# Performance work log

Hardware: AMD Instinct MI355X
Metric: run time of the kernel (lower is better)

The kernel has to match this reference:

```python
import jax, jax.numpy as jnp
import numpy as np

B, C, D, H, W = 2, 64, 8, 24, 24  # hidden_dim = C; N = D*H*W = 4608 tokens


def setup_inputs() -> dict:
    key = jax.random.key(0)
    ks = jax.random.split(key, 8)
    s = 1.0 / np.sqrt(C)  # fan-in style init for 1x1 conv weights
    return {
        "x": jax.random.normal(ks[0], (B, C, D, H, W), dtype=jnp.float32),
        "h": jax.random.normal(ks[1], (B, C, D, H, W), dtype=jnp.float32),
        "Wq": jax.random.normal(ks[2], (C, C), dtype=jnp.float32) * s,
        "bq": jax.random.normal(ks[3], (C,), dtype=jnp.float32) * s,
        "Wk": jax.random.normal(ks[4], (C, C), dtype=jnp.float32) * s,
        "bk": jax.random.normal(ks[5], (C,), dtype=jnp.float32) * s,
        "Wv": jax.random.normal(ks[6], (C, C), dtype=jnp.float32) * s,
        "bv": jax.random.normal(ks[7], (C,), dtype=jnp.float32) * s,
    }


def reference(x, h, Wq, bq, Wk, bk, Wv, bv):
    # 1x1 Conv3d == per-token linear over channels
    def proj(inp, Wt, bt):
        f = inp.reshape(inp.shape[0], inp.shape[1], -1)  # [B, C, N]
        return jnp.einsum('oc,bcn->bon', Wt, f) + bt[None, :, None]

    q = proj(x, Wq, bq)  # [B, C, N]
    k = proj(h, Wk, bk)  # [B, C, N]
    v = proj(h, Wv, bv)  # [B, C, N]

    scale = 1.0 / np.sqrt(k.shape[1])  # k.size(1) ** 0.5 == sqrt(C)
    scores = jnp.einsum('bcm,bcn->bmn', q, k) * scale  # [B, N, N]
    attn = jax.nn.softmax(scores, axis=-1)
    out = jnp.einsum('bcn,bmn->bcm', v, attn)  # [B, C, N]
    return out.reshape(h.shape)
```

## Files before the change

### kernel.cpp

```cpp
#include <hip/hip_runtime.h>
#include <hip/hip_bf16.h>

#define C_DIM 64
#define N_TOK 4608
#define NBLK  72
#define B_SZ  2
#define MTILES 288
#define NSEG  8
#define SEGLEN (N_TOK / NSEG)
#define KTILES 288
#define VTILES 72

typedef __bf16 bf16x8 __attribute__((ext_vector_type(8)));
typedef float  f32x4  __attribute__((ext_vector_type(4)));


__device__ __forceinline__ void gemm_tile(
    const __hip_bfloat16* wmat, const bf16x8 bin[2], const float* bias,
    int col, int quad, f32x4 acc[4])
{
    #pragma unroll
    for (int ot = 0; ot < 4; ot++) {
        f32x4 a = (f32x4){0.f, 0.f, 0.f, 0.f};
        #pragma unroll
        for (int kh = 0; kh < 2; kh++) {
            bf16x8 wf = *(const bf16x8*)(wmat + (ot * 16 + col) * 72 +
                                         kh * 32 + quad * 8);
            a = __builtin_amdgcn_mfma_f32_16x16x32_bf16(wf, bin[kh], a, 0, 0, 0);
        }
        float4 b4 = *(const float4*)(bias + ot * 16 + quad * 4);
        a[0] += b4.x; a[1] += b4.y; a[2] += b4.z; a[3] += b4.w;
        acc[ot] = a;
    }
}

__device__ __forceinline__ void store_swz(
    __hip_bfloat16* dst, const f32x4 acc[4], int col, int quad, float sc)
{
    #pragma unroll
    for (int ot = 0; ot < 4; ot++) {
        union { __hip_bfloat16 e[4]; uint2 v; } pk;
        #pragma unroll
        for (int r = 0; r < 4; r++) pk.e[r] = __float2bfloat16(acc[ot][r] * sc);
        *(uint2*)(dst + (ot >> 1) * 512 + ((ot * 2 + (quad >> 1)) & 3) * 128 +
                  col * 8 + (quad & 1) * 4) = pk.v;
    }
}

__global__ __launch_bounds__(256) void proj_kernel(
    const float* __restrict__ x,  const float* __restrict__ h,
    const float* __restrict__ Wq, const float* __restrict__ bq,
    const float* __restrict__ Wk, const float* __restrict__ bk,
    const float* __restrict__ Wv, const float* __restrict__ bv,
    __hip_bfloat16* __restrict__ qS, __hip_bfloat16* __restrict__ kS,
    __hip_bfloat16* __restrict__ vS)
{
    __shared__ __hip_bfloat16 wl[3 * 64 * 72];
    __shared__ __hip_bfloat16 xt[64 * 72];
    __shared__ __hip_bfloat16 ht[64 * 72];
    __shared__ __hip_bfloat16 vl[64 * 72];

    const int b  = blockIdx.x / NBLK;
    const int n0 = (blockIdx.x % NBLK) * 64;
    const int t  = threadIdx.x;

    #pragma unroll
    for (int mat = 0; mat < 3; mat++) {
        const float* W = (mat == 0) ? Wq : ((mat == 1) ? Wk : Wv);
        __hip_bfloat16* wd = wl + mat * (64 * 72);
        #pragma unroll
        for (int i = 0; i < 16; i++) {
            const int idx = i * 256 + t;
            wd[(idx >> 6) * 72 + (idx & 63)] = __float2bfloat16(W[idx]);
        }
    }
    #pragma unroll
    for (int i = 0; i < 16; i++) {
        const int idx = i * 256 + t;
        const int c = idx >> 6, n = idx & 63;
        xt[n * 72 + c] = __float2bfloat16(x[(size_t)(b * C_DIM + c) * N_TOK + n0 + n]);
        ht[n * 72 + c] = __float2bfloat16(h[(size_t)(b * C_DIM + c) * N_TOK + n0 + n]);
    }
    __syncthreads();

    const int wave = t >> 6, lane = t & 63;
    const int col = lane & 15, quad = lane >> 4;

    bf16x8 xb[2], hb[2];
    #pragma unroll
    for (int kh = 0; kh < 2; kh++) {
        xb[kh] = *(const bf16x8*)(xt + (wave * 16 + col) * 72 + kh * 32 + quad * 8);
        hb[kh] = *(const bf16x8*)(ht + (wave * 16 + col) * 72 + kh * 32 + quad * 8);
    }

    const size_t tile16 = (size_t)b * KTILES + (n0 >> 4) + wave;
    f32x4 acc[4];

    gemm_tile(wl + 0 * (64 * 72), xb, bq, col, quad, acc);
    store_swz(qS + (tile16 << 10), acc, col, quad, 0.125f * 1.44269504088896f);

    gemm_tile(wl + 1 * (64 * 72), hb, bk, col, quad, acc);
    store_swz(kS + (tile16 << 10), acc, col, quad, 1.0f);

    gemm_tile(wl + 2 * (64 * 72), hb, bv, col, quad, acc);
    #pragma unroll
    for (int ot = 0; ot < 4; ot++)
        #pragma unroll
        for (int r = 0; r < 4; r++)
            vl[(ot * 16 + quad * 4 + r) * 72 + wave * 16 + col] =
                __float2bfloat16(acc[ot][r]);
    __syncthreads();
    {
        const size_t vbase = ((size_t)(b * VTILES) + (n0 >> 6)) << 12;
        #pragma unroll
        for (int rep = 0; rep < 2; rep++) {
            const int ch = rep * 256 + t;
            const int cc = ch >> 7, hf = (ch >> 6) & 1;
            const int qd = (ch >> 4) & 3, c2 = ch & 15;
            *(uint4*)(vS + vbase + (size_t)ch * 8) =
                *(const uint4*)(vl + (cc * 16 + c2) * 72 + hf * 32 + qd * 8);
        }
    }
}

__global__ __launch_bounds__(512, 4) void attn_kernel(
    const __hip_bfloat16* __restrict__ qS,
    const __hip_bfloat16* __restrict__ kS,
    const __hip_bfloat16* __restrict__ vS,
    float* __restrict__ out)
{
    __shared__ __hip_bfloat16 plds[NSEG * 16 * 72];
    __shared__ float o_lds[NSEG * 16 * 64];
    __shared__ float mstat[NSEG][16];
    __shared__ float lstat[NSEG][16];

    const int b    = blockIdx.x / MTILES;
    const int mblk = blockIdx.x % MTILES;
    const int wave = threadIdx.x >> 6;
    const int lane = threadIdx.x & 63;
    const int col  = lane & 15;
    const int quad = lane >> 4;
    const int m0   = mblk * 16;

    __hip_bfloat16* pw = plds + wave * (16 * 72);

    const __hip_bfloat16* qp =
        qS + (((size_t)b * KTILES + (m0 >> 4)) << 10) + lane * 8;
    const bf16x8 qf0 = *(const bf16x8*)(qp);
    const bf16x8 qf1 = *(const bf16x8*)(qp + 512);

    f32x4 accO[4];
    #pragma unroll
    for (int cc = 0; cc < 4; cc++) accO[cc] = (f32x4){0.f, 0.f, 0.f, 0.f};
    float rmax = -3.0e38f, rsum = 0.f;

    const int nbeg = wave * SEGLEN;

    #pragma unroll 1
    for (int n0 = nbeg; n0 < nbeg + SEGLEN; n0 += 64) {
        const __hip_bfloat16* vt =
            vS + ((((size_t)b * VTILES) + (n0 >> 6)) << 12) + lane * 8;
        bf16x8 va[8];
        #pragma unroll
        for (int cc = 0; cc < 4; cc++) {
            va[2 * cc]     = *(const bf16x8*)(vt + cc * 1024);
            va[2 * cc + 1] = *(const bf16x8*)(vt + cc * 1024 + 512);
        }

        const __hip_bfloat16* kt =
            kS + (((size_t)b * KTILES + (n0 >> 4)) << 10) + lane * 8;
        f32x4 s[4];
        #pragma unroll
        for (int j = 0; j < 4; j++) {
            bf16x8 ka0 = *(const bf16x8*)(kt + (j << 10));
            bf16x8 ka1 = *(const bf16x8*)(kt + (j << 10) + 512);
            s[j] = __builtin_amdgcn_mfma_f32_16x16x32_bf16(
                       ka0, qf0, (f32x4){0.f, 0.f, 0.f, 0.f}, 0, 0, 0);
            s[j] = __builtin_amdgcn_mfma_f32_16x16x32_bf16(ka1, qf1, s[j], 0, 0, 0);
        }

        float tm = s[0][0];
        #pragma unroll
        for (int j = 0; j < 4; j++)
            #pragma unroll
            for (int r = 0; r < 4; r++) tm = fmaxf(tm, s[j][r]);
        tm = fmaxf(tm, __shfl_xor(tm, 16));
        tm = fmaxf(tm, __shfl_xor(tm, 32));
        const float nmax  = fmaxf(rmax, tm);
        const float alpha = __builtin_amdgcn_exp2f(rmax - nmax);
        rmax = nmax;

        float pv[16];
        float psum = 0.f;
        #pragma unroll
        for (int j = 0; j < 4; j++)
            #pragma unroll
            for (int r = 0; r < 4; r++) {
                float e = __builtin_amdgcn_exp2f(s[j][r] - nmax);
                pv[j * 4 + r] = e;
                psum += e;
            }
        rsum = rsum * alpha + psum;

        #pragma unroll
        for (int cc = 0; cc < 4; cc++)
            #pragma unroll
            for (int r = 0; r < 4; r++) accO[cc][r] *= alpha;

        #pragma unroll
        for (int j = 0; j < 4; j++) {
            union { __hip_bfloat16 e[4]; uint2 v; } pk;
            #pragma unroll
            for (int r = 0; r < 4; r++) pk.e[r] = __float2bfloat16(pv[j * 4 + r]);
            *(uint2*)(pw + col * 72 + j * 16 + quad * 4) = pk.v;
        }
        __asm__ volatile("s_waitcnt lgkmcnt(0)" ::: "memory");

        const bf16x8 pb0 = *(const bf16x8*)(pw + col * 72 + quad * 8);
        const bf16x8 pb1 = *(const bf16x8*)(pw + col * 72 + 32 + quad * 8);
        #pragma unroll
        for (int cc = 0; cc < 4; cc++) {
            accO[cc] = __builtin_amdgcn_mfma_f32_16x16x32_bf16(va[2 * cc],     pb0, accO[cc], 0, 0, 0);
            accO[cc] = __builtin_amdgcn_mfma_f32_16x16x32_bf16(va[2 * cc + 1], pb1, accO[cc], 0, 0, 0);
        }
    }

    rsum += __shfl_xor(rsum, 16);
    rsum += __shfl_xor(rsum, 32);
    #pragma unroll
    for (int cc = 0; cc < 4; cc++)
        *(f32x4*)(o_lds + (wave * 16 + col) * 64 + cc * 16 + quad * 4) = accO[cc];
    if (quad == 0) { mstat[wave][col] = rmax; lstat[wave][col] = rsum; }
    __syncthreads();

    if (threadIdx.x < 256) {
        const int m  = threadIdx.x & 15;
        const int cq = threadIdx.x >> 4;
        float M = -3.0e38f;
        #pragma unroll
        for (int sgm = 0; sgm < NSEG; sgm++) M = fmaxf(M, mstat[sgm][m]);
        float lsum = 0.f;
        f32x4 oacc = (f32x4){0.f, 0.f, 0.f, 0.f};
        #pragma unroll
        for (int sgm = 0; sgm < NSEG; sgm++) {
            const float w = __builtin_amdgcn_exp2f(mstat[sgm][m] - M);
            lsum += w * lstat[sgm][m];
            oacc += w * *(const f32x4*)(o_lds + (sgm * 16 + m) * 64 + cq * 4);
        }
        const float inv = 1.0f / lsum;
        #pragma unroll
        for (int r = 0; r < 4; r++) {
            const int c = cq * 4 + r;
            out[(size_t)(b * C_DIM + c) * N_TOK + m0 + m] = oacc[r] * inv;
        }
    }
}

extern "C" void kernel_launch(void* const* d_in, const int* in_sizes, int n_in,
                              void* d_out, int out_size, void* d_ws, size_t ws_size,
                              hipStream_t stream) {
    const float* x  = (const float*)d_in[0];
    const float* h  = (const float*)d_in[1];
    const float* Wq = (const float*)d_in[2];
    const float* bq = (const float*)d_in[3];
    const float* Wk = (const float*)d_in[4];
    const float* bk = (const float*)d_in[5];
    const float* Wv = (const float*)d_in[6];
    const float* bv = (const float*)d_in[7];
    float* out = (float*)d_out;

    const size_t elems = (size_t)B_SZ * N_TOK * C_DIM;
    __hip_bfloat16* qS = (__hip_bfloat16*)d_ws;
    __hip_bfloat16* kS = qS + elems;
    __hip_bfloat16* vS = kS + elems;

    proj_kernel<<<B_SZ * NBLK, 256, 0, stream>>>(x, h, Wq, bq, Wk, bk, Wv, bv,
                                                 qS, kS, vS);
    attn_kernel<<<B_SZ * MTILES, 512, 0, stream>>>(qS, kS, vS, out);
}
```

Baseline: 106.6 us.

## Process two query tiles per attention block and vectorize projection loads

Each attention block now handles 32 query rows (two 16-row tiles) instead of 16, so every K and V fragment loaded from global memory feeds twice as many MFMAs. This halves the grid to 288 blocks and raises register pressure from the doubled accumulators and score tiles. The final merge is done in two phases, with an output LDS stride padded to 68 to reduce bank conflicts. The projection kernel switches to float4 global loads for the weights and activations.

```diff
diff --git a/kernel.cpp b/kernel.cpp
--- a/kernel.cpp
+++ b/kernel.cpp
@@ -5,11 +5,12 @@
 #define N_TOK 4608
 #define NBLK  72
 #define B_SZ  2
-#define MTILES 288
+#define MBLKS 144
 #define NSEG  8
 #define SEGLEN (N_TOK / NSEG)
 #define KTILES 288
 #define VTILES 72
+#define OSTR  68
 
 typedef __bf16 bf16x8 __attribute__((ext_vector_type(8)));
 typedef float  f32x4  __attribute__((ext_vector_type(4)));
@@ -69,17 +70,30 @@
         const float* W = (mat == 0) ? Wq : ((mat == 1) ? Wk : Wv);
         __hip_bfloat16* wd = wl + mat * (64 * 72);
         #pragma unroll
-        for (int i = 0; i < 16; i++) {
-            const int idx = i * 256 + t;
-            wd[(idx >> 6) * 72 + (idx & 63)] = __float2bfloat16(W[idx]);
-        }
-    }
-    #pragma unroll
-    for (int i = 0; i < 16; i++) {
-        const int idx = i * 256 + t;
-        const int c = idx >> 6, n = idx & 63;
-        xt[n * 72 + c] = __float2bfloat16(x[(size_t)(b * C_DIM + c) * N_TOK + n0 + n]);
-        ht[n * 72 + c] = __float2bfloat16(h[(size_t)(b * C_DIM + c) * N_TOK + n0 + n]);
+        for (int i = 0; i < 4; i++) {
+            const int ch = i * 256 + t;
+            const int o = ch >> 4, c0 = (ch & 15) * 4;
+            float4 w4 = *(const float4*)(W + ch * 4);
+            union { __hip_bfloat16 e[4]; uint2 v; } pk;
+            pk.e[0] = __float2bfloat16(w4.x); pk.e[1] = __float2bfloat16(w4.y);
+            pk.e[2] = __float2bfloat16(w4.z); pk.e[3] = __float2bfloat16(w4.w);
+            *(uint2*)(wd + o * 72 + c0) = pk.v;
+        }
+    }
+    #pragma unroll
+    for (int i = 0; i < 4; i++) {
+        const int ch = i * 256 + t;
+        const int c = ch >> 4, n4 = (ch & 15) * 4;
+        float4 x4 = *(const float4*)(x + (size_t)(b * C_DIM + c) * N_TOK + n0 + n4);
+        float4 h4 = *(const float4*)(h + (size_t)(b * C_DIM + c) * N_TOK + n0 + n4);
+        xt[(n4 + 0) * 72 + c] = __float2bfloat16(x4.x);
+        xt[(n4 + 1) * 72 + c] = __float2bfloat16(x4.y);
+        xt[(n4 + 2) * 72 + c] = __float2bfloat16(x4.z);
+        xt[(n4 + 3) * 72 + c] = __float2bfloat16(x4.w);
+        ht[(n4 + 0) * 72 + c] = __float2bfloat16(h4.x);
+        ht[(n4 + 1) * 72 + c] = __float2bfloat16(h4.y);
+        ht[(n4 + 2) * 72 + c] = __float2bfloat16(h4.z);
+        ht[(n4 + 3) * 72 + c] = __float2bfloat16(h4.w);
     }
     __syncthreads();
 
@@ -129,35 +143,121 @@
     const __hip_bfloat16* __restrict__ vS,
     float* __restrict__ out)
 {
-    __shared__ __hip_bfloat16 plds[NSEG * 16 * 72];
-    __shared__ float o_lds[NSEG * 16 * 64];
-    __shared__ float mstat[NSEG][16];
-    __shared__ float lstat[NSEG][16];
-
-    const int b    = blockIdx.x / MTILES;
-    const int mblk = blockIdx.x % MTILES;
+    __shared__ __hip_bfloat16 plds[NSEG * 2 * 16 * 72];
+    __shared__ float o_lds[NSEG * 16 * OSTR];
+    __shared__ float mstat[NSEG][32];
+    __shared__ float lstat[NSEG][32];
+
+    const int b    = blockIdx.x / MBLKS;
+    const int mblk = blockIdx.x % MBLKS;
     const int wave = threadIdx.x >> 6;
     const int lane = threadIdx.x & 63;
     const int col  = lane & 15;
     const int quad = lane >> 4;
-    const int m0   = mblk * 16;
-
-    __hip_bfloat16* pw = plds + wave * (16 * 72);
+    const int m0   = mblk * 32;
+
+    __hip_bfloat16* pw0 = plds + wave * (2 * 16 * 72);
+    __hip_bfloat16* pw1 = pw0 + 16 * 72;
 
     const __hip_bfloat16* qp =
         qS + (((size_t)b * KTILES + (m0 >> 4)) << 10) + lane * 8;
-    const bf16x8 qf0 = *(const bf16x8*)(qp);
-    const bf16x8 qf1 = *(const bf16x8*)(qp + 512);
-
-    f32x4 accO[4];
-    #pragma unroll
-    for (int cc = 0; cc < 4; cc++) accO[cc] = (f32x4){0.f, 0.f, 0.f, 0.f};
-    float rmax = -3.0e38f, rsum = 0.f;
+    const bf16x8 qa0 = *(const bf16x8*)(qp);
+    const bf16x8 qa1 = *(const bf16x8*)(qp + 512);
+    const bf16x8 qb0 = *(const bf16x8*)(qp + 1024);
+    const bf16x8 qb1 = *(const bf16x8*)(qp + 1536);
+
+    f32x4 accO0[4], accO1[4];
+    #pragma unroll
+    for (int cc = 0; cc < 4; cc++) {
+        accO0[cc] = (f32x4){0.f, 0.f, 0.f, 0.f};
+        accO1[cc] = (f32x4){0.f, 0.f, 0.f, 0.f};
+    }
+    float rmax0 = -3.0e38f, rsum0 = 0.f;
+    float rmax1 = -3.0e38f, rsum1 = 0.f;
 
     const int nbeg = wave * SEGLEN;
 
     #pragma unroll 1
     for (int n0 = nbeg; n0 < nbeg + SEGLEN; n0 += 64) {
+        const __hip_bfloat16* kt =
+            kS + (((size_t)b * KTILES + (n0 >> 4)) << 10) + lane * 8;
+        bf16x8 ka[8];
+        #pragma unroll
+        for (int j = 0; j < 4; j++) {
+            ka[2 * j]     = *(const bf16x8*)(kt + (j << 10));
+            ka[2 * j + 1] = *(const bf16x8*)(kt + (j << 10) + 512);
+        }
+
+        f32x4 s0[4], s1[4];
+        #pragma unroll
+        for (int j = 0; j < 4; j++) {
+            s0[j] = __builtin_amdgcn_mfma_f32_16x16x32_bf16(
+                        ka[2 * j], qa0, (f32x4){0.f, 0.f, 0.f, 0.f}, 0, 0, 0);
+            s0[j] = __builtin_amdgcn_mfma_f32_16x16x32_bf16(ka[2 * j + 1], qa1, s0[j], 0, 0, 0);
+            s1[j] = __builtin_amdgcn_mfma_f32_16x16x32_bf16(
+                        ka[2 * j], qb0, (f32x4){0.f, 0.f, 0.f, 0.f}, 0, 0, 0);
+            s1[j] = __builtin_amdgcn_mfma_f32_16x16x32_bf16(ka[2 * j + 1], qb1, s1[j], 0, 0, 0);
+        }
+
+        {
+            float tm = s0[0][0];
+            #pragma unroll
+            for (int j = 0; j < 4; j++)
+                #pragma unroll
+                for (int r = 0; r < 4; r++) tm = fmaxf(tm, s0[j][r]);
+            tm = fmaxf(tm, __shfl_xor(tm, 16));
+            tm = fmaxf(tm, __shfl_xor(tm, 32));
+            const float nmax  = fmaxf(rmax0, tm);
+            const float alpha = __builtin_amdgcn_exp2f(rmax0 - nmax);
+            rmax0 = nmax;
+            float psum = 0.f;
+            #pragma unroll
+            for (int j = 0; j < 4; j++) {
+                union { __hip_bfloat16 e[4]; uint2 v; } pk;
+                #pragma unroll
+                for (int r = 0; r < 4; r++) {
+                    float e = __builtin_amdgcn_exp2f(s0[j][r] - nmax);
+                    psum += e;
+                    pk.e[r] = __float2bfloat16(e);
+                }
+                *(uint2*)(pw0 + col * 72 + j * 16 + quad * 4) = pk.v;
+            }
+            rsum0 = rsum0 * alpha + psum;
+            #pragma unroll
+            for (int cc = 0; cc < 4; cc++)
+                #pragma unroll
+                for (int r = 0; r < 4; r++) accO0[cc][r] *= alpha;
+        }
+        {
+            float tm = s1[0][0];
+            #pragma unroll
+            for (int j = 0; j < 4; j++)
+                #pragma unroll
+                for (int r = 0; r < 4; r++) tm = fmaxf(tm, s1[j][r]);
+            tm = fmaxf(tm, __shfl_xor(tm, 16));
+            tm = fmaxf(tm, __shfl_xor(tm, 32));
+            const float nmax  = fmaxf(rmax1, tm);
+            const float alpha = __builtin_amdgcn_exp2f(rmax1 - nmax);
+            rmax1 = nmax;
+            float psum = 0.f;
+            #pragma unroll
+            for (int j = 0; j < 4; j++) {
+                union { __hip_bfloat16 e[4]; uint2 v; } pk;
+                #pragma unroll
+                for (int r = 0; r < 4; r++) {
+                    float e = __builtin_amdgcn_exp2f(s1[j][r] - nmax);
+                    psum += e;
+                    pk.e[r] = __float2bfloat16(e);
+                }
+                *(uint2*)(pw1 + col * 72 + j * 16 + quad * 4) = pk.v;
+            }
+            rsum1 = rsum1 * alpha + psum;
+            #pragma unroll
+            for (int cc = 0; cc < 4; cc++)
+                #pragma unroll
+                for (int r = 0; r < 4; r++) accO1[cc][r] *= alpha;
+        }
+
         const __hip_bfloat16* vt =
             vS + ((((size_t)b * VTILES) + (n0 >> 6)) << 12) + lane * 8;
         bf16x8 va[8];
@@ -166,93 +266,60 @@
             va[2 * cc]     = *(const bf16x8*)(vt + cc * 1024);
             va[2 * cc + 1] = *(const bf16x8*)(vt + cc * 1024 + 512);
         }
-
-        const __hip_bfloat16* kt =
-            kS + (((size_t)b * KTILES + (n0 >> 4)) << 10) + lane * 8;
-        f32x4 s[4];
-        #pragma unroll
-        for (int j = 0; j < 4; j++) {
-            bf16x8 ka0 = *(const bf16x8*)(kt + (j << 10));
-            bf16x8 ka1 = *(const bf16x8*)(kt + (j << 10) + 512);
-            s[j] = __builtin_amdgcn_mfma_f32_16x16x32_bf16(
-                       ka0, qf0, (f32x4){0.f, 0.f, 0.f, 0.f}, 0, 0, 0);
-            s[j] = __builtin_amdgcn_mfma_f32_16x16x32_bf16(ka1, qf1, s[j], 0, 0, 0);
-        }
-
-        float tm = s[0][0];
-        #pragma unroll
-        for (int j = 0; j < 4; j++)
-            #pragma unroll
-            for (int r = 0; r < 4; r++) tm = fmaxf(tm, s[j][r]);
-        tm = fmaxf(tm, __shfl_xor(tm, 16));
-        tm = fmaxf(tm, __shfl_xor(tm, 32));
-        const float nmax  = fmaxf(rmax, tm);
-        const float alpha = __builtin_amdgcn_exp2f(rmax - nmax);
-        rmax = nmax;
-
-        float pv[16];
-        float psum = 0.f;
-        #pragma unroll
-        for (int j = 0; j < 4; j++)
+        __asm__ volatile("s_waitcnt lgkmcnt(0)" ::: "memory");
+
+        const bf16x8 p00 = *(const bf16x8*)(pw0 + col * 72 + quad * 8);
+        const bf16x8 p01 = *(const bf16x8*)(pw0 + col * 72 + 32 + quad * 8);
+        const bf16x8 p10 = *(const bf16x8*)(pw1 + col * 72 + quad * 8);
+        const bf16x8 p11 = *(const bf16x8*)(pw1 + col * 72 + 32 + quad * 8);
+        #pragma unroll
+        for (int cc = 0; cc < 4; cc++) {
+            accO0[cc] = __builtin_amdgcn_mfma_f32_16x16x32_bf16(va[2 * cc],     p00, accO0[cc], 0, 0, 0);
+            accO0[cc] = __builtin_amdgcn_mfma_f32_16x16x32_bf16(va[2 * cc + 1], p01, accO0[cc], 0, 0, 0);
+            accO1[cc] = __builtin_amdgcn_mfma_f32_16x16x32_bf16(va[2 * cc],     p10, accO1[cc], 0, 0, 0);
+            accO1[cc] = __builtin_amdgcn_mfma_f32_16x16x32_bf16(va[2 * cc + 1], p11, accO1[cc], 0, 0, 0);
+        }
+    }
+
+    rsum0 += __shfl_xor(rsum0, 16);  rsum0 += __shfl_xor(rsum0, 32);
+    rsum1 += __shfl_xor(rsum1, 16);  rsum1 += __shfl_xor(rsum1, 32);
+    if (quad == 0) {
+        mstat[wave][col]      = rmax0;  lstat[wave][col]      = rsum0;
+        mstat[wave][16 + col] = rmax1;  lstat[wave][16 + col] = rsum1;
+    }
+
+    #pragma unroll
+    for (int phase = 0; phase < 2; phase++) {
+        const f32x4* accp = phase ? accO1 : accO0;
+        #pragma unroll
+        for (int cc = 0; cc < 4; cc++)
+            *(f32x4*)(o_lds + (wave * 16 + col) * OSTR + cc * 16 + quad * 4) =
+                accp[cc];
+        __syncthreads();
+        if (threadIdx.x < 256) {
+            const int m  = threadIdx.x & 15;
+            const int cq = threadIdx.x >> 4;
+            const int mi = phase * 16 + m;
+            float M = -3.0e38f;
+            #pragma unroll
+            for (int sgm = 0; sgm < NSEG; sgm++) M = fmaxf(M, mstat[sgm][mi]);
+            float lsum = 0.f;
+            f32x4 oacc = (f32x4){0.f, 0.f, 0.f, 0.f};
+            #pragma unroll
+            for (int sgm = 0; sgm < NSEG; sgm++) {
+                const float w = __builtin_amdgcn_exp2f(mstat[sgm][mi] - M);
+                lsum += w * lstat[sgm][mi];
+                oacc += w * *(const f32x4*)(o_lds + (sgm * 16 + m) * OSTR + cq * 4);
+            }
+            const float inv = 1.0f / lsum;
             #pragma unroll
             for (int r = 0; r < 4; r++) {
-                float e = __builtin_amdgcn_exp2f(s[j][r] - nmax);
-                pv[j * 4 + r] = e;
-                psum += e;
+                const int c = cq * 4 + r;
+                out[(size_t)(b * C_DIM + c) * N_TOK + m0 + phase * 16 + m] =
+                    oacc[r] * inv;
             }
-        rsum = rsum * alpha + psum;
-
-        #pragma unroll
-        for (int cc = 0; cc < 4; cc++)
-            #pragma unroll
-            for (int r = 0; r < 4; r++) accO[cc][r] *= alpha;
-
-        #pragma unroll
-        for (int j = 0; j < 4; j++) {
-            union { __hip_bfloat16 e[4]; uint2 v; } pk;
-            #pragma unroll
-            for (int r = 0; r < 4; r++) pk.e[r] = __float2bfloat16(pv[j * 4 + r]);
-            *(uint2*)(pw + col * 72 + j * 16 + quad * 4) = pk.v;
-        }
-        __asm__ volatile("s_waitcnt lgkmcnt(0)" ::: "memory");
-
-        const bf16x8 pb0 = *(const bf16x8*)(pw + col * 72 + quad * 8);
-        const bf16x8 pb1 = *(const bf16x8*)(pw + col * 72 + 32 + quad * 8);
-        #pragma unroll
-        for (int cc = 0; cc < 4; cc++) {
-            accO[cc] = __builtin_amdgcn_mfma_f32_16x16x32_bf16(va[2 * cc],     pb0, accO[cc], 0, 0, 0);
-            accO[cc] = __builtin_amdgcn_mfma_f32_16x16x32_bf16(va[2 * cc + 1], pb1, accO[cc], 0, 0, 0);
-        }
-    }
-
-    rsum += __shfl_xor(rsum, 16);
-    rsum += __shfl_xor(rsum, 32);
-    #pragma unroll
-    for (int cc = 0; cc < 4; cc++)
-        *(f32x4*)(o_lds + (wave * 16 + col) * 64 + cc * 16 + quad * 4) = accO[cc];
-    if (quad == 0) { mstat[wave][col] = rmax; lstat[wave][col] = rsum; }
-    __syncthreads();
-
-    if (threadIdx.x < 256) {
-        const int m  = threadIdx.x & 15;
-        const int cq = threadIdx.x >> 4;
-        float M = -3.0e38f;
-        #pragma unroll
-        for (int sgm = 0; sgm < NSEG; sgm++) M = fmaxf(M, mstat[sgm][m]);
-        float lsum = 0.f;
-        f32x4 oacc = (f32x4){0.f, 0.f, 0.f, 0.f};
-        #pragma unroll
-        for (int sgm = 0; sgm < NSEG; sgm++) {
-            const float w = __builtin_amdgcn_exp2f(mstat[sgm][m] - M);
-            lsum += w * lstat[sgm][m];
-            oacc += w * *(const f32x4*)(o_lds + (sgm * 16 + m) * 64 + cq * 4);
-        }
-        const float inv = 1.0f / lsum;
-        #pragma unroll
-        for (int r = 0; r < 4; r++) {
-            const int c = cq * 4 + r;
-            out[(size_t)(b * C_DIM + c) * N_TOK + m0 + m] = oacc[r] * inv;
-        }
+        }
+        __syncthreads();
     }
 }
 
@@ -276,5 +343,5 @@
 
     proj_kernel<<<B_SZ * NBLK, 256, 0, stream>>>(x, h, Wq, bq, Wk, bk, Wv, bv,
                                                  qS, kS, vS);
-    attn_kernel<<<B_SZ * MTILES, 512, 0, stream>>>(qS, kS, vS, out);
-}
+    attn_kernel<<<B_SZ * MBLKS, 512, 0, stream>>>(qS, kS, vS, out);
+}
```

Result: no change. 104.6 us (-1.9%).
